# Performance work log

Measured on AMD Instinct MI355X. Metric: run time of the kernel, lower is better.

Reference implementation:

```python
import jax, jax.numpy as jnp
import numpy as np

N_NEIGHBORS = 5


def setup_inputs() -> dict:
    key = jax.random.key(0)
    k1, k2, k3 = jax.random.split(key, 3)
    B, N, D = 2048, 100000, 128
    x = jax.random.normal(k1, (B, D), dtype=jnp.float32)
    train_data = jax.random.normal(k2, (N, D), dtype=jnp.float32)
    train_labels = jax.random.normal(k3, (N,), dtype=jnp.float32)
    return {"x": x, "train_data": train_data, "train_labels": train_labels}


def reference(x, train_data, train_labels):
    # Euclidean (minkowski p=2) pairwise distances [B, N] via the GEMM
    x2 = jnp.sum(x * x, axis=1, keepdims=True)            # [B,1]
    t2 = jnp.sum(train_data * train_data, axis=1)          # [N]
    d2 = x2 - 2.0 * (x @ train_data.T) + t2[None, :]       # [B,N]
    dist = jnp.sqrt(jnp.maximum(d2, 0.0))

    # k smallest distances (torch.topk largest=False)
    neg_d, idx = jax.lax.top_k(-dist, N_NEIGHBORS)         # [B,k]
    d = -neg_d

    labels = train_labels[idx]                             # [B,k]

    # weights = 'distance': inverse distance, with exact-match handling
    d_inv = 1.0 / d
    inf_mask = jnp.isinf(d_inv)
    inf_row = jnp.any(inf_mask, axis=1, keepdims=True)
    w = jnp.where(inf_row, inf_mask.astype(jnp.float32), d_inv)  # [B,k]

    out = jnp.sum(w * labels, axis=1) / jnp.sum(w, axis=1)  # [B]
    return out
```

## Files before the change

kernel.cpp:

```cpp
#include <hip/hip_runtime.h>
#include <math.h>

typedef __attribute__((ext_vector_type(8))) int   i32x8;
typedef __attribute__((ext_vector_type(4))) float f32x4;
typedef unsigned int uint32;
typedef unsigned char uchar;

#define KNN_K   5
#define DIM     128
#define FLT_BIG 3.402823466e38f
#define KEY_C   512.0f

#define MF_B     2048
#define MF_N     100000
#define MF_QPB   256
#define MF_QPW   64
#define MF_NCH   256
#define MF_CHS   400
#define MF_NPAD  (MF_NCH * MF_CHS)
#define MF_CSLOT 4
#define MF_NCAND (MF_NCH * MF_CSLOT)
#define MF_RESCORE 16
#define SCALE1   0x7F7F7F7Fu

__device__ __forceinline__ uint32 umn(uint32 a, uint32 b) { return a < b ? a : b; }
__device__ __forceinline__ uint32 umx(uint32 a, uint32 b) { return a > b ? a : b; }

#define TOP5_INSERT(v, id)                                                  \
    if ((v) < bd4) {                                                        \
        bool l0 = (v) < bd0, l1 = (v) < bd1, l2 = (v) < bd2, l3 = (v) < bd3;\
        if (l3) { bd4 = bd3; bi4 = bi3; } else { bd4 = (v); bi4 = (id); }   \
        if (l2) { bd3 = bd2; bi3 = bi2; } else if (l3) { bd3 = (v); bi3 = (id); } \
        if (l1) { bd2 = bd1; bi2 = bi1; } else if (l2) { bd2 = (v); bi2 = (id); } \
        if (l0) { bd1 = bd0; bi1 = bi0; } else if (l1) { bd1 = (v); bi1 = (id); } \
        if (l0) { bd0 = (v); bi0 = (id); }                                  \
    }

#if defined(__has_builtin) && __has_builtin(__builtin_amdgcn_cvt_pk_fp8_f32)
#define HAVE_CVT_FP8 1
#else
#define HAVE_CVT_FP8 0
__device__ __forceinline__ uint32 f2fp8_u(float f) {
    uint32 u = __float_as_uint(f);
    uint32 s = (u >> 31) << 7;
    uint32 au = u & 0x7FFFFFFFu;
    float a = __uint_as_float(au);
    if (a >= 448.f) return s | 0x7Eu;
    int ex = (int)((au >> 23) & 0xFF) - 127;
    if (ex < -6) {
        int m = (int)(a * 512.f + 0.5f);
        return s | (uint32)(m > 7 ? 7 : m);
    }
    uint32 r = au + 0x7FFFFu + ((au >> 20) & 1u);
    ex = (int)((r >> 23) & 0xFF) - 127;
    if (ex > 8) return s | 0x7Eu;
    return s | ((uint32)(ex + 7) << 3) | ((r >> 20) & 7u);
}
#endif

__global__ __launch_bounds__(256) void prep_kernel(
        const float* __restrict__ train, const float* __restrict__ x,
        uchar* __restrict__ tf8, uchar* __restrict__ xf8,
        float* __restrict__ t2c) {
    const int wv = threadIdx.x >> 6, lane = threadIdx.x & 63;
    const int tblocks = MF_NPAD / 64;
    const bool isx = (blockIdx.x >= tblocks);
    const int blk = isx ? (blockIdx.x - tblocks) : blockIdx.x;
    const int row = (blk * 4 + wv) * 16 + (lane >> 2);

    const float* src; uchar* dst;
    if (isx) {
        if (row >= MF_B) return;
        src = x; dst = xf8;
    } else {
        if (row >= MF_N) {
            if (row < MF_NPAD && (lane & 3) == 0) t2c[row] = -1e30f;
            return;
        }
        src = train; dst = tf8;
    }
    const int seg = (lane & 3) * 32;
    const float4* p = (const float4*)(src + (size_t)row * DIM + seg);

    float4 v[8];
#pragma unroll
    for (int j = 0; j < 8; ++j) v[j] = p[j];

    uint32 d[8];
#pragma unroll
    for (int j = 0; j < 8; ++j) {
#if HAVE_CVT_FP8
        int r = __builtin_amdgcn_cvt_pk_fp8_f32(v[j].x, v[j].y, 0, false);
        r = __builtin_amdgcn_cvt_pk_fp8_f32(v[j].z, v[j].w, r, true);
        d[j] = (uint32)r;
#else
        d[j] = f2fp8_u(v[j].x) | (f2fp8_u(v[j].y) << 8)
             | (f2fp8_u(v[j].z) << 16) | (f2fp8_u(v[j].w) << 24);
#endif
    }
    uint4* o = (uint4*)(dst + (size_t)row * DIM + seg);
    o[0] = make_uint4(d[0], d[1], d[2], d[3]);
    o[1] = make_uint4(d[4], d[5], d[6], d[7]);

    if (!isx) {
        float s = 0.f;
#pragma unroll
        for (int j = 0; j < 8; ++j)
            s += v[j].x * v[j].x + v[j].y * v[j].y + v[j].z * v[j].z + v[j].w * v[j].w;
        s += __shfl_xor(s, 1);
        s += __shfl_xor(s, 2);
        if ((lane & 3) == 0) t2c[row] = -(s + KEY_C) * 0.5f;
    }
}

__global__ __launch_bounds__(256, 4) void knn_mfma(
        const uchar* __restrict__ xf8, const uchar* __restrict__ tf8,
        const float* __restrict__ t2c, uint32* __restrict__ cand_k) {
    __shared__ uint32 sk[4][MF_QPW][12];

    const int id   = blockIdx.x;
    const int r8   = id & 7, g = id >> 3;
    const int chunk = ((g >> 3) << 3) | r8;
    const int jq   = g & 7;
    const int tid  = threadIdx.x;
    const int wv   = tid >> 6;
    const int lane = tid & 63;
    const int quad = lane >> 4;
    const int c16  = lane & 15;
    const int qbase = jq * MF_QPB + wv * MF_QPW;
    const int n0 = chunk * MF_CHS;

    i32x8 bq[4];
#pragma unroll
    for (int t = 0; t < 4; ++t)
        bq[t] = *(const i32x8*)(xf8 + (size_t)(qbase + t * 16 + c16) * DIM
                                + quad * 32);

    uint32 L0[4], L1[4], L2[4];
#pragma unroll
    for (int t = 0; t < 4; ++t) { L0[t] = 0xFFFFFFFFu; L1[t] = 0xFFFFFFFFu; L2[t] = 0xFFFFFFFFu; }

    const uchar* ap = tf8 + (size_t)(n0 + c16) * DIM + quad * 32;
    const float* tp = t2c + n0 + quad * 4;

    auto process = [&](i32x8 F, float4 tv, uint32 r0) {
#pragma unroll
        for (int t = 0; t < 4; ++t) {
            f32x4 acc = (f32x4){tv.x, tv.y, tv.z, tv.w};
            acc = __builtin_amdgcn_mfma_scale_f32_16x16x128_f8f6f4(
                      F, bq[t], acc, 0, 0, 0, (int)SCALE1, 0, (int)SCALE1);
            uint32 p0 = (__float_as_uint(acc[0]) & 0xFFFFFC00u) | r0;
            uint32 p1 = (__float_as_uint(acc[1]) & 0xFFFFFC00u) | (r0 + 1);
            uint32 p2 = (__float_as_uint(acc[2]) & 0xFFFFFC00u) | (r0 + 2);
            uint32 p3 = (__float_as_uint(acc[3]) & 0xFFFFFC00u) | (r0 + 3);
            uint32 m0 = umn(p0, p1), M0 = umx(p0, p1);
            uint32 m1 = umn(p2, p3), M1 = umx(p2, p3);
            uint32 s0 = umn(m0, m1);
            uint32 s1 = umn(umx(m0, m1), umn(M0, M1));
            uint32 a0 = L0[t], a1 = L1[t], a2 = L2[t];
            uint32 m  = umn(a0, s0);
            uint32 M  = umx(a0, s0);
            uint32 n  = umn(a1, s1);
            uint32 N  = umx(a1, s1);
            uint32 l1 = umn(M, n);
            uint32 P  = umx(M, n);
            L0[t] = m;
            L1[t] = l1;
            L2[t] = umn(umn(P, N), a2);
        }
    };

    i32x8 fa, fb;
    float4 tva, tvb;
    fa = *(const i32x8*)ap;
    tva = *(const float4*)tp;

    uint32 r0 = (uint32)(quad * 4);
    for (int it = 0; it < 12; ++it) {
        fb = *(const i32x8*)(ap + 16 * DIM);
        tvb = *(const float4*)(tp + 16);
        process(fa, tva, r0);
        fa = *(const i32x8*)(ap + 32 * DIM);
        tva = *(const float4*)(tp + 32);
        process(fb, tvb, r0 + 16);
        ap += 32 * DIM; tp += 32; r0 += 32;
    }
    process(fa, tva, r0);

#pragma unroll
    for (int t = 0; t < 4; ++t) {
        sk[wv][t * 16 + c16][quad * 3 + 0] = L0[t];
        sk[wv][t * 16 + c16][quad * 3 + 1] = L1[t];
        sk[wv][t * 16 + c16][quad * 3 + 2] = L2[t];
    }
    __syncthreads();

    const int mw = tid >> 6, ml = tid & 63;
    uint32 k0 = 0xFFFFFFFFu, k1 = 0xFFFFFFFFu, k2 = 0xFFFFFFFFu, k3 = 0xFFFFFFFFu;
#pragma unroll
    for (int j = 0; j < 12; ++j) {
        uint32 v = sk[mw][ml][j];
        uint32 t0 = umx(k0, v);
        k0 = umn(k0, v);
        uint32 t1 = umx(k1, t0);
        k1 = umn(k1, t0);
        uint32 t2_ = umx(k2, t1);
        k2 = umn(k2, t1);
        k3 = umn(k3, t2_);
    }
    const size_t base = ((size_t)(jq * MF_QPB + tid) * MF_NCH + chunk) * MF_CSLOT;
    uint4 kk; kk.x = k0; kk.y = k1; kk.z = k2; kk.w = k3;
    *(uint4*)(cand_k + base) = kk;
}

__global__ __launch_bounds__(256) void knn_final(
        const uint32* __restrict__ cand_k,
        const float* __restrict__ x, const float* __restrict__ train,
        const float* __restrict__ labels, float* __restrict__ out) {
    const int q = blockIdx.x * 4 + (threadIdx.x >> 6);
    const int lane = threadIdx.x & 63;
    const float xa = x[(size_t)q * DIM + lane];
    const float xb = x[(size_t)q * DIM + 64 + lane];

    uint32 ck[16]; uint32 cid[16];
    const size_t cb = (size_t)q * MF_NCAND;
#pragma unroll
    for (int j = 0; j < 16; ++j) {
        const int p = lane + 64 * j;
        uint32 k = cand_k[cb + p];
        ck[j] = k;
        cid[j] = (uint32)(p >> 2) * MF_CHS + (k & 1023u);
    }

    uint32 selid[MF_RESCORE];
    uint32 tk = 0, ti = 0; bool first = true;
#pragma unroll
    for (int round = 0; round < MF_RESCORE; ++round) {
        uint32 mk = 0xFFFFFFFFu, mi = 0xFFFFFFFFu;
#pragma unroll
        for (int j = 0; j < 16; ++j) {
            bool gt = first || (ck[j] > tk) || (ck[j] == tk && cid[j] > ti);
            if (gt && ((ck[j] < mk) || (ck[j] == mk && cid[j] < mi))) {
                mk = ck[j]; mi = cid[j];
            }
        }
#pragma unroll
        for (int off = 32; off; off >>= 1) {
            uint32 ok = __shfl_xor(mk, off);
            uint32 oi = __shfl_xor(mi, off);
            if (ok < mk || (ok == mk && oi < mi)) { mk = ok; mi = oi; }
        }
        selid[round] = mi;
        tk = mk; ti = mi; first = false;
    }

    float d2v[MF_RESCORE];
#pragma unroll
    for (int r = 0; r < MF_RESCORE; ++r) {
        const float* tr = train + (size_t)selid[r] * DIM;
        float da = xa - tr[lane];
        float db = xb - tr[64 + lane];
        d2v[r] = fmaf(da, da, db * db);
    }
#pragma unroll
    for (int r = 0; r < MF_RESCORE; ++r) {
#pragma unroll
        for (int off = 32; off; off >>= 1) d2v[r] += __shfl_xor(d2v[r], off);
    }

    float bd0 = FLT_BIG, bd1 = FLT_BIG, bd2 = FLT_BIG, bd3 = FLT_BIG, bd4 = FLT_BIG;
    int   bi0 = 0, bi1 = 0, bi2 = 0, bi3 = 0, bi4 = 0;
#pragma unroll
    for (int r = 0; r < MF_RESCORE; ++r) {
        float v = d2v[r]; int id = (int)selid[r];
        TOP5_INSERT(v, id);
    }

    float d0 = sqrtf(fmaxf(bd0, 0.f));
    float d1 = sqrtf(fmaxf(bd1, 0.f));
    float d2_ = sqrtf(fmaxf(bd2, 0.f));
    float d3 = sqrtf(fmaxf(bd3, 0.f));
    float d4 = sqrtf(fmaxf(bd4, 0.f));
    bool zero = (d0 == 0.f) || (d1 == 0.f) || (d2_ == 0.f) || (d3 == 0.f) || (d4 == 0.f);
    float w0, w1, w2, w3, w4;
    if (zero) {
        w0 = (d0 == 0.f) ? 1.f : 0.f;
        w1 = (d1 == 0.f) ? 1.f : 0.f;
        w2 = (d2_ == 0.f) ? 1.f : 0.f;
        w3 = (d3 == 0.f) ? 1.f : 0.f;
        w4 = (d4 == 0.f) ? 1.f : 0.f;
    } else {
        w0 = 1.f / d0; w1 = 1.f / d1; w2 = 1.f / d2_; w3 = 1.f / d3; w4 = 1.f / d4;
    }
    float wsum = w0 + w1 + w2 + w3 + w4;
    float lsum = w0 * labels[bi0] + w1 * labels[bi1] + w2 * labels[bi2]
               + w3 * labels[bi3] + w4 * labels[bi4];
    if (lane == 0) out[q] = lsum / wsum;
}

#define FB_QT     16
#define FB_NCHUNK 25
#define FB_NT     256

__global__ void rowsq_kernel(const float* __restrict__ data,
                             float* __restrict__ out, int rows) {
    int r = blockIdx.x * blockDim.x + threadIdx.x;
    if (r >= rows) return;
    const float4* p = (const float4*)(data + (size_t)r * DIM);
    float s0 = 0.f, s1 = 0.f, s2 = 0.f, s3 = 0.f;
#pragma unroll
    for (int i = 0; i < DIM / 4; ++i) {
        float4 v = p[i];
        s0 += v.x * v.x; s1 += v.y * v.y; s2 += v.z * v.z; s3 += v.w * v.w;
    }
    out[r] = (s0 + s1) + (s2 + s3);
}

__global__ __launch_bounds__(FB_NT) void fb_phaseA(
        const float* __restrict__ x, const float* __restrict__ train,
        const float* __restrict__ x2, const float* __restrict__ t2,
        float* __restrict__ cand_d, int* __restrict__ cand_i,
        int N, int chunkSize) {
    __shared__ float xs[FB_QT][DIM + 4];
    __shared__ float rd[FB_QT][16 * KNN_K];
    __shared__ int   ri[FB_QT][16 * KNN_K];

    const int q0 = blockIdx.x * FB_QT;
    const int chunk = blockIdx.y;
    const int n0 = chunk * chunkSize;
    const int n1 = min(n0 + chunkSize, N);
    const int t = threadIdx.x;

    for (int i = t; i < FB_QT * DIM; i += FB_NT) {
        int q = i >> 7, d = i & (DIM - 1);
        xs[q][d] = x[(size_t)(q0 + q) * DIM + d];
    }
    __syncthreads();

    const int q  = t & (FB_QT - 1);
    const int ln = t >> 4;
    const float myx2 = x2[q0 + q];
    const float4* xp = (const float4*)xs[q];

    float bd0 = FLT_BIG, bd1 = FLT_BIG, bd2 = FLT_BIG, bd3 = FLT_BIG, bd4 = FLT_BIG;
    int   bi0 = -1, bi1 = -1, bi2 = -1, bi3 = -1, bi4 = -1;

    int n = n0 + ln;
    for (; n < n1; n += 16) {
        const float4* r0 = (const float4*)(train + (size_t)n * DIM);
        float dA = 0.f;
#pragma unroll 8
        for (int i = 0; i < DIM / 4; ++i) {
            float4 a = xp[i], b0 = r0[i];
            dA += a.x * b0.x + a.y * b0.y + a.z * b0.z + a.w * b0.w;
        }
        float vA = myx2 - 2.f * dA + t2[n];
        TOP5_INSERT(vA, n);
    }

    rd[q][ln * KNN_K + 0] = bd0;  ri[q][ln * KNN_K + 0] = bi0;
    rd[q][ln * KNN_K + 1] = bd1;  ri[q][ln * KNN_K + 1] = bi1;
    rd[q][ln * KNN_K + 2] = bd2;  ri[q][ln * KNN_K + 2] = bi2;
    rd[q][ln * KNN_K + 3] = bd3;  ri[q][ln * KNN_K + 3] = bi3;
    rd[q][ln * KNN_K + 4] = bd4;  ri[q][ln * KNN_K + 4] = bi4;
    __syncthreads();

    if (t < FB_QT) {
        float* dq = rd[t]; int* iq = ri[t];
        size_t base = ((size_t)(q0 + t) * FB_NCHUNK + chunk) * KNN_K;
#pragma unroll
        for (int k = 0; k < KNN_K; ++k) {
            float best = FLT_BIG; int bj = 0;
            for (int j = 0; j < 16 * KNN_K; ++j) {
                float v = dq[j];
                if (v < best) { best = v; bj = j; }
            }
            cand_d[base + k] = best; cand_i[base + k] = iq[bj];
            dq[bj] = FLT_BIG;
        }
    }
}

__global__ void fb_phaseB(const float* __restrict__ cand_d,
                          const int* __restrict__ cand_i,
                          const float* __restrict__ labels,
                          float* __restrict__ out, int B, int ncand) {
    int qq = blockIdx.x * blockDim.x + threadIdx.x;
    if (qq >= B) return;
    const float* cd = cand_d + (size_t)qq * ncand;
    const int*   ci = cand_i + (size_t)qq * ncand;

    float bd0 = FLT_BIG, bd1 = FLT_BIG, bd2 = FLT_BIG, bd3 = FLT_BIG, bd4 = FLT_BIG;
    int   bi0 = -1, bi1 = -1, bi2 = -1, bi3 = -1, bi4 = -1;
    for (int j = 0; j < ncand; ++j) {
        float v = cd[j]; int id = ci[j];
        TOP5_INSERT(v, id);
    }
    float d0 = sqrtf(fmaxf(bd0, 0.f));
    float d1 = sqrtf(fmaxf(bd1, 0.f));
    float d2 = sqrtf(fmaxf(bd2, 0.f));
    float d3 = sqrtf(fmaxf(bd3, 0.f));
    float d4 = sqrtf(fmaxf(bd4, 0.f));
    bool zero = (d0 == 0.f) || (d1 == 0.f) || (d2 == 0.f) || (d3 == 0.f) || (d4 == 0.f);
    float w0, w1, w2, w3, w4;
    if (zero) {
        w0 = (d0 == 0.f) ? 1.f : 0.f;
        w1 = (d1 == 0.f) ? 1.f : 0.f;
        w2 = (d2 == 0.f) ? 1.f : 0.f;
        w3 = (d3 == 0.f) ? 1.f : 0.f;
        w4 = (d4 == 0.f) ? 1.f : 0.f;
    } else {
        w0 = 1.f / d0; w1 = 1.f / d1; w2 = 1.f / d2; w3 = 1.f / d3; w4 = 1.f / d4;
    }
    float wsum = w0 + w1 + w2 + w3 + w4;
    float lsum = w0 * labels[bi0] + w1 * labels[bi1] + w2 * labels[bi2]
               + w3 * labels[bi3] + w4 * labels[bi4];
    out[qq] = lsum / wsum;
}

static inline size_t align256(size_t v) { return (v + 255) & ~(size_t)255; }

extern "C" void kernel_launch(void* const* d_in, const int* in_sizes, int n_in,
                              void* d_out, int out_size, void* d_ws, size_t ws_size,
                              hipStream_t stream) {
    const float* x      = (const float*)d_in[0];
    const float* train  = (const float*)d_in[1];
    const float* labels = (const float*)d_in[2];

    const int N = in_sizes[2];
    const int D = in_sizes[1] / N;
    const int B = in_sizes[0] / D;
    (void)n_in;

    size_t o_tf8 = 0;
    size_t o_xf8 = align256(o_tf8 + (size_t)MF_NPAD * DIM);
    size_t o_t2c = align256(o_xf8 + (size_t)B * DIM);
    size_t o_ck  = align256(o_t2c + (size_t)MF_NPAD * sizeof(float));
    size_t need  = align256(o_ck + (size_t)B * MF_NCAND * sizeof(uint32));

    const bool mfma_ok = (N == MF_N) && (D == DIM) && (B == MF_B) && (ws_size >= need);

    if (mfma_ok) {
        uchar* tf8 = (uchar*)d_ws + o_tf8;
        uchar* xf8 = (uchar*)d_ws + o_xf8;
        float* t2c = (float*)((char*)d_ws + o_t2c);
        uint32* cand_k = (uint32*)((char*)d_ws + o_ck);

        prep_kernel<<<MF_NPAD / 64 + MF_B / 64, 256, 0, stream>>>(
            train, x, tf8, xf8, t2c);
        knn_mfma<<<MF_NCH * 8, 256, 0, stream>>>(xf8, tf8, t2c, cand_k);
        knn_final<<<MF_B / 4, 256, 0, stream>>>(cand_k, x, train, labels,
                                                (float*)d_out);
    } else {
        float* t2     = (float*)d_ws;
        float* x2v    = t2 + N;
        float* cand_d = x2v + B;
        int*   cand_i = (int*)(cand_d + (size_t)B * FB_NCHUNK * KNN_K);

        rowsq_kernel<<<(N + 255) / 256, 256, 0, stream>>>(train, t2, N);
        rowsq_kernel<<<(B + 255) / 256, 256, 0, stream>>>(x, x2v, B);
        const int chunkSize = (N + FB_NCHUNK - 1) / FB_NCHUNK;
        dim3 gridA(B / FB_QT, FB_NCHUNK);
        fb_phaseA<<<gridA, FB_NT, 0, stream>>>(x, train, x2v, t2,
                                               cand_d, cand_i, N, chunkSize);
        fb_phaseB<<<(B + 255) / 256, 256, 0, stream>>>(cand_d, cand_i, labels,
                                                       (float*)d_out, B,
                                                       FB_NCHUNK * KNN_K);
    }
}
```

Before: 191.1 us.

## Batch eight MFMAs per step and prefetch two tiles ahead in knn_mfma

Restructures the main loop of the distance kernel so eight scaled FP8 MFMAs (two 16-row tiles × four query groups) are issued back-to-back before the min-network reductions. The next two tiles are prefetched while those reductions run. The aim is to hide MFMA latency and global-load latency behind the top-3 selection ALU work. Keeping more accumulators live raises register pressure, so launch bounds drop to 3 waves per SIMD and occupancy falls. Workspace slack is added because the last iteration's prefetch reads past the chunk end.

```diff
diff --git a/kernel.cpp b/kernel.cpp
--- a/kernel.cpp
+++ b/kernel.cpp
@@ -18,6 +18,7 @@
 #define MF_NCH   256
 #define MF_CHS   400
 #define MF_NPAD  (MF_NCH * MF_CHS)
+#define MF_SLACK 32
 #define MF_CSLOT 4
 #define MF_NCAND (MF_NCH * MF_CSLOT)
 #define MF_RESCORE 16
@@ -113,7 +114,7 @@
     }
 }
 
-__global__ __launch_bounds__(256, 4) void knn_mfma(
+__global__ __launch_bounds__(256, 3) void knn_mfma(
         const uchar* __restrict__ xf8, const uchar* __restrict__ tf8,
         const float* __restrict__ t2c, uint32* __restrict__ cand_k) {
     __shared__ uint32 sk[4][MF_QPW][12];
@@ -143,49 +144,83 @@
     const uchar* ap = tf8 + (size_t)(n0 + c16) * DIM + quad * 32;
     const float* tp = t2c + n0 + quad * 4;
 
-    auto process = [&](i32x8 F, float4 tv, uint32 r0) {
-#pragma unroll
-        for (int t = 0; t < 4; ++t) {
-            f32x4 acc = (f32x4){tv.x, tv.y, tv.z, tv.w};
-            acc = __builtin_amdgcn_mfma_scale_f32_16x16x128_f8f6f4(
-                      F, bq[t], acc, 0, 0, 0, (int)SCALE1, 0, (int)SCALE1);
-            uint32 p0 = (__float_as_uint(acc[0]) & 0xFFFFFC00u) | r0;
-            uint32 p1 = (__float_as_uint(acc[1]) & 0xFFFFFC00u) | (r0 + 1);
-            uint32 p2 = (__float_as_uint(acc[2]) & 0xFFFFFC00u) | (r0 + 2);
-            uint32 p3 = (__float_as_uint(acc[3]) & 0xFFFFFC00u) | (r0 + 3);
-            uint32 m0 = umn(p0, p1), M0 = umx(p0, p1);
-            uint32 m1 = umn(p2, p3), M1 = umx(p2, p3);
-            uint32 s0 = umn(m0, m1);
-            uint32 s1 = umn(umx(m0, m1), umn(M0, M1));
-            uint32 a0 = L0[t], a1 = L1[t], a2 = L2[t];
-            uint32 m  = umn(a0, s0);
-            uint32 M  = umx(a0, s0);
-            uint32 n  = umn(a1, s1);
-            uint32 N  = umx(a1, s1);
-            uint32 l1 = umn(M, n);
-            uint32 P  = umx(M, n);
-            L0[t] = m;
-            L1[t] = l1;
-            L2[t] = umn(umn(P, N), a2);
-        }
+    auto net = [&](f32x4 acc, uint32 r0, int t) {
+        uint32 p0 = (__float_as_uint(acc[0]) & 0xFFFFFC00u) | r0;
+        uint32 p1 = (__float_as_uint(acc[1]) & 0xFFFFFC00u) | (r0 + 1);
+        uint32 p2 = (__float_as_uint(acc[2]) & 0xFFFFFC00u) | (r0 + 2);
+        uint32 p3 = (__float_as_uint(acc[3]) & 0xFFFFFC00u) | (r0 + 3);
+        uint32 m0 = umn(p0, p1), M0 = umx(p0, p1);
+        uint32 m1 = umn(p2, p3), M1 = umx(p2, p3);
+        uint32 s0 = umn(m0, m1);
+        uint32 s1 = umn(umx(m0, m1), umn(M0, M1));
+        uint32 a0 = L0[t], a1 = L1[t], a2 = L2[t];
+        uint32 m  = umn(a0, s0);
+        uint32 M  = umx(a0, s0);
+        uint32 n  = umn(a1, s1);
+        uint32 N  = umx(a1, s1);
+        uint32 l1 = umn(M, n);
+        uint32 P  = umx(M, n);
+        L0[t] = m;
+        L1[t] = l1;
+        L2[t] = umn(umn(P, N), a2);
     };
 
-    i32x8 fa, fb;
-    float4 tva, tvb;
-    fa = *(const i32x8*)ap;
-    tva = *(const float4*)tp;
+    #define MFMA8(accA, accB, FA, FB, TA, TB)                               \
+        _Pragma("unroll")                                                   \
+        for (int t = 0; t < 4; ++t)                                         \
+            accA[t] = __builtin_amdgcn_mfma_scale_f32_16x16x128_f8f6f4(     \
+                FA, bq[t], (f32x4){TA.x, TA.y, TA.z, TA.w},                 \
+                0, 0, 0, (int)SCALE1, 0, (int)SCALE1);                      \
+        _Pragma("unroll")                                                   \
+        for (int t = 0; t < 4; ++t)                                         \
+            accB[t] = __builtin_amdgcn_mfma_scale_f32_16x16x128_f8f6f4(     \
+                FB, bq[t], (f32x4){TB.x, TB.y, TB.z, TB.w},                 \
+                0, 0, 0, (int)SCALE1, 0, (int)SCALE1);
+
+    i32x8  fa = *(const i32x8*)ap;
+    i32x8  fb = *(const i32x8*)(ap + 16 * DIM);
+    i32x8  fc, fd;
+    float4 tva = *(const float4*)tp;
+    float4 tvb = *(const float4*)(tp + 16);
+    float4 tvc, tvd;
 
     uint32 r0 = (uint32)(quad * 4);
-    for (int it = 0; it < 12; ++it) {
-        fb = *(const i32x8*)(ap + 16 * DIM);
-        tvb = *(const float4*)(tp + 16);
-        process(fa, tva, r0);
-        fa = *(const i32x8*)(ap + 32 * DIM);
-        tva = *(const float4*)(tp + 32);
-        process(fb, tvb, r0 + 16);
-        ap += 32 * DIM; tp += 32; r0 += 32;
-    }
-    process(fa, tva, r0);
+    for (int it = 0; it < 6; ++it) {
+        f32x4 aA[4], aB[4];
+        MFMA8(aA, aB, fa, fb, tva, tvb)
+        fc  = *(const i32x8*)(ap + 32 * DIM);
+        fd  = *(const i32x8*)(ap + 48 * DIM);
+        tvc = *(const float4*)(tp + 32);
+        tvd = *(const float4*)(tp + 48);
+#pragma unroll
+        for (int t = 0; t < 4; ++t) net(aA[t], r0, t);
+#pragma unroll
+        for (int t = 0; t < 4; ++t) net(aB[t], r0 + 16, t);
+
+        f32x4 aC[4], aD[4];
+        MFMA8(aC, aD, fc, fd, tvc, tvd)
+        fa  = *(const i32x8*)(ap + 64 * DIM);
+        fb  = *(const i32x8*)(ap + 80 * DIM);
+        tva = *(const float4*)(tp + 64);
+        tvb = *(const float4*)(tp + 80);
+#pragma unroll
+        for (int t = 0; t < 4; ++t) net(aC[t], r0 + 32, t);
+#pragma unroll
+        for (int t = 0; t < 4; ++t) net(aD[t], r0 + 48, t);
+
+        ap += 64 * DIM; tp += 64; r0 += 64;
+    }
+    {
+        f32x4 aA[4];
+#pragma unroll
+        for (int t = 0; t < 4; ++t)
+            aA[t] = __builtin_amdgcn_mfma_scale_f32_16x16x128_f8f6f4(
+                        fa, bq[t], (f32x4){tva.x, tva.y, tva.z, tva.w},
+                        0, 0, 0, (int)SCALE1, 0, (int)SCALE1);
+#pragma unroll
+        for (int t = 0; t < 4; ++t) net(aA[t], r0, t);
+    }
+    #undef MFMA8
 
 #pragma unroll
     for (int t = 0; t < 4; ++t) {
@@ -433,9 +468,9 @@
     (void)n_in;
 
     size_t o_tf8 = 0;
-    size_t o_xf8 = align256(o_tf8 + (size_t)MF_NPAD * DIM);
+    size_t o_xf8 = align256(o_tf8 + (size_t)(MF_NPAD + MF_SLACK) * DIM);
     size_t o_t2c = align256(o_xf8 + (size_t)B * DIM);
-    size_t o_ck  = align256(o_t2c + (size_t)MF_NPAD * sizeof(float));
+    size_t o_ck  = align256(o_t2c + (size_t)(MF_NPAD + MF_SLACK) * sizeof(float));
     size_t need  = align256(o_ck + (size_t)B * MF_NCAND * sizeof(uint32));
 
     const bool mfma_ok = (N == MF_N) && (D == DIM) && (B == MF_B) && (ws_size >= need);
```

After: 191.8 us. About the same (+0.4%).
